# Optimization experiments

Hardware: AMD Instinct MI355X
Metric: run time of the kernel (lower is better)

Reference implementation:

```python
import jax, jax.numpy as jnp
import numpy as np

MOV_DIM = 16
HID = 128
N_MOV = 500_000
N_PHASE = 125_000
N_EDGE = 1_000_000


def setup_inputs() -> dict:
    key = jax.random.key(0)
    ks = jax.random.split(key, 16)
    s_in = 1.0 / np.sqrt(MOV_DIM)
    s_h = 1.0 / np.sqrt(HID)
    inp = {
        "x_movement": jax.random.normal(ks[0], (N_MOV, MOV_DIM), jnp.float32),
        "W1": jax.random.normal(ks[1], (MOV_DIM, HID), jnp.float32) * s_in,
        "b1": jnp.full((HID,), 0.01, jnp.float32),
        "W2": jax.random.normal(ks[2], (HID, HID), jnp.float32) * s_h,
        "b2": jnp.full((HID,), 0.01, jnp.float32),
        "W3": jax.random.normal(ks[3], (HID, HID), jnp.float32) * s_h,
        "b3": jnp.full((HID,), 0.01, jnp.float32),
        "W4": jax.random.normal(ks[4], (HID, HID), jnp.float32) * s_h,
        "b4": jnp.full((HID,), 0.01, jnp.float32),
        "W5": jax.random.normal(ks[5], (HID, HID), jnp.float32) * s_h,
        "b5": jnp.full((HID,), 0.01, jnp.float32),
        "W6": jax.random.normal(ks[6], (HID, 1), jnp.float32) * s_h,
        "b6": jnp.full((1,), 0.01, jnp.float32),
        "edge_src": jax.random.randint(ks[7], (N_EDGE,), 0, N_MOV, jnp.int32),
        "edge_dst": jax.random.randint(ks[8], (N_EDGE,), 0, N_PHASE, jnp.int32),
        "n_phases": N_PHASE,
    }
    return inp


def reference(x_movement, W1, b1, W2, b2, W3, b3, W4, b4, W5, b5, W6, b6,
              edge_src, edge_dst, n_phases):
    h = jax.nn.relu(x_movement @ W1 + b1)
    h = jax.nn.relu(h @ W2 + b2)
    h = jax.nn.relu(h @ W3 + b3)
    # scatter-mean aggregation movement -> phase over edge list
    msg = h[edge_src]                                   # [E, HID] gather
    ssum = jax.ops.segment_sum(msg, edge_dst, num_segments=n_phases)
    cnt = jax.ops.segment_sum(jnp.ones((edge_dst.shape[0],), h.dtype),
                              edge_dst, num_segments=n_phases)
    agg = ssum / jnp.maximum(cnt, 1.0)[:, None]          # [N_phase, HID]
    # phase MLP -> logits
    p = jax.nn.relu(agg @ W4 + b4)
    p = jax.nn.relu(p @ W5 + b5)
    logits = (p @ W6 + b6).squeeze(-1)                  # [N_phase]
    return logits
```

## Files before the change

kernel.cpp:

```cpp
#include <hip/hip_runtime.h>
#include <hip/hip_bf16.h>


typedef __attribute__((ext_vector_type(8))) short short8;
typedef __attribute__((ext_vector_type(4))) float f32x4;

union U8 { short8 s8; unsigned int u[4]; };

__device__ __forceinline__ float bf2f(unsigned short u) {
  return __uint_as_float(((unsigned int)u) << 16);
}
__device__ __forceinline__ unsigned short f2bf(float f) {
  unsigned int u = __float_as_uint(f);
  u = (u + 0x7fffu + ((u >> 16) & 1u)) >> 16;
  return (unsigned short)u;
}
__device__ __forceinline__ unsigned int pk2(float a, float b) {
  __hip_bfloat162 h = __float22bfloat162_rn(make_float2(a, b));
  unsigned int u;
  __builtin_memcpy(&u, &h, 4);
  return u;
}

__global__ __launch_bounds__(256)
void prep_weights(const float* __restrict__ W1, const float* __restrict__ W2,
                  const float* __restrict__ W3, const float* __restrict__ W4,
                  const float* __restrict__ W5,
                  unsigned short* __restrict__ w1t, unsigned short* __restrict__ w2t,
                  unsigned short* __restrict__ w3t, unsigned short* __restrict__ w4t,
                  unsigned short* __restrict__ w5t) {
  int t = blockIdx.x * blockDim.x + threadIdx.x;
  int stride = gridDim.x * blockDim.x;
  if (t < 128 * 32) {
    int c = t >> 5, k = t & 31;
    w1t[t] = (k < 16) ? f2bf(W1[k * 128 + c]) : 0;
  }
  for (int i = t; i < 128 * 128; i += stride) {
    int c = i >> 7, k = i & 127;
    w2t[i] = f2bf(W2[k * 128 + c]);
    w3t[i] = f2bf(W3[k * 128 + c]);
    w4t[i] = f2bf(W4[k * 128 + c]);
    w5t[i] = f2bf(W5[k * 128 + c]);
  }
}

__device__ __forceinline__
void mov_tile(int rowBlk, unsigned short* sH,
              const float* __restrict__ x,
              const unsigned short* __restrict__ w1t,
              const unsigned short* __restrict__ w2t,
              const unsigned short* __restrict__ w3t,
              const float* __restrict__ b1, const float* __restrict__ b2,
              const float* __restrict__ b3,
              unsigned short* __restrict__ hout, int nrows) {
  const int tid  = threadIdx.x;
  const int lane = tid & 63;
  const int w    = tid >> 6;
  const int li   = lane & 15;
  const int g    = lane >> 4;
  const int r0w  = (w & 1) * 32;
  const int c0   = (w >> 1) * 64;

  f32x4 acc[2][4];
  short8 Bf[4][4];

#pragma unroll
  for (int cf = 0; cf < 4; ++cf) {
    float4 b4 = *(const float4*)&b1[c0 + cf * 16 + g * 4];
#pragma unroll
    for (int rf = 0; rf < 2; ++rf) {
      acc[rf][cf][0] = b4.x; acc[rf][cf][1] = b4.y;
      acc[rf][cf][2] = b4.z; acc[rf][cf][3] = b4.w;
    }
  }
  {
    short8 Ax[2];
#pragma unroll
    for (int rf = 0; rf < 2; ++rf) {
      U8 a; a.s8 = (short8)0;
      int row = rowBlk + r0w + rf * 16 + li;
      if (g < 2 && row < nrows) {
        const float* xp = x + (size_t)row * 16 + g * 8;
        float4 u0 = *(const float4*)xp;
        float4 u1 = *(const float4*)(xp + 4);
        a.u[0] = pk2(u0.x, u0.y); a.u[1] = pk2(u0.z, u0.w);
        a.u[2] = pk2(u1.x, u1.y); a.u[3] = pk2(u1.z, u1.w);
      }
      Ax[rf] = a.s8;
    }
    short8 B1[4];
#pragma unroll
    for (int cf = 0; cf < 4; ++cf)
      B1[cf] = *(const short8*)&w1t[(c0 + cf * 16 + li) * 32 + g * 8];
#pragma unroll
    for (int rf = 0; rf < 2; ++rf)
#pragma unroll
      for (int cf = 0; cf < 4; ++cf)
        acc[rf][cf] = __builtin_amdgcn_mfma_f32_16x16x32_bf16(B1[cf], Ax[rf], acc[rf][cf], 0, 0, 0);
  }

#pragma unroll
  for (int rf = 0; rf < 2; ++rf) {
    int s = r0w + rf * 16 + li;
    unsigned short* dst = &sH[s * 128 + (g & 1) * 4];
    int sx = s & 7;
#pragma unroll
    for (int cf = 0; cf < 4; ++cf) {
      int gi = (c0 >> 3) + cf * 2 + (g >> 1);
      int slot = gi ^ sx;
      uint2 u;
      u.x = pk2(fmaxf(acc[rf][cf][0], 0.f), fmaxf(acc[rf][cf][1], 0.f));
      u.y = pk2(fmaxf(acc[rf][cf][2], 0.f), fmaxf(acc[rf][cf][3], 0.f));
      *(uint2*)(dst + slot * 8) = u;
    }
  }
  __syncthreads();

  const unsigned short* wts[2] = { w2t, w3t };
  const float* bs[2] = { b2, b3 };
#pragma unroll 1
  for (int layer = 0; layer < 2; ++layer) {
    const unsigned short* wt = wts[layer];
    const float* bb = bs[layer];
#pragma unroll
    for (int ks = 0; ks < 4; ++ks)
#pragma unroll
      for (int cf = 0; cf < 4; ++cf)
        Bf[ks][cf] = *(const short8*)&wt[(c0 + cf * 16 + li) * 128 + ks * 32 + g * 8];

#pragma unroll
    for (int cf = 0; cf < 4; ++cf) {
      float4 b4 = *(const float4*)&bb[c0 + cf * 16 + g * 4];
#pragma unroll
      for (int rf = 0; rf < 2; ++rf) {
        acc[rf][cf][0] = b4.x; acc[rf][cf][1] = b4.y;
        acc[rf][cf][2] = b4.z; acc[rf][cf][3] = b4.w;
      }
    }

#pragma unroll
    for (int ks = 0; ks < 4; ++ks) {
      short8 Ar[2];
#pragma unroll
      for (int rf = 0; rf < 2; ++rf) {
        int s = r0w + rf * 16 + li;
        int slot = (ks * 4 + g) ^ (s & 7);
        Ar[rf] = *(const short8*)&sH[s * 128 + slot * 8];
      }
#pragma unroll
      for (int rf = 0; rf < 2; ++rf)
#pragma unroll
        for (int cf = 0; cf < 4; ++cf)
          acc[rf][cf] = __builtin_amdgcn_mfma_f32_16x16x32_bf16(Bf[ks][cf], Ar[rf], acc[rf][cf], 0, 0, 0);
    }
    __syncthreads();

#pragma unroll
    for (int rf = 0; rf < 2; ++rf) {
      int s = r0w + rf * 16 + li;
      unsigned short* dst = &sH[s * 128 + (g & 1) * 4];
      int sx = s & 7;
#pragma unroll
      for (int cf = 0; cf < 4; ++cf) {
        int gi = (c0 >> 3) + cf * 2 + (g >> 1);
        int slot = gi ^ sx;
        uint2 u;
        u.x = pk2(fmaxf(acc[rf][cf][0], 0.f), fmaxf(acc[rf][cf][1], 0.f));
        u.y = pk2(fmaxf(acc[rf][cf][2], 0.f), fmaxf(acc[rf][cf][3], 0.f));
        *(uint2*)(dst + slot * 8) = u;
      }
    }
    __syncthreads();
  }

  {
    int r = tid >> 2;
    int q = tid & 3;
    int grow = rowBlk + r;
    if (grow < nrows) {
#pragma unroll
      for (int i = 0; i < 4; ++i) {
        int gi = q * 4 + i;
        int slot = gi ^ (r & 7);
        short8 v = *(const short8*)&sH[r * 128 + slot * 8];
        *(short8*)(hout + (size_t)grow * 128 + gi * 8) = v;
      }
    }
  }
}

__device__ __forceinline__ bool role_other(int b, int k, int otherB, int* oIdx, int* mIdx) {
  bool other = ((b % k) == (k - 1)) && ((b / k) < otherB);
  *oIdx = b / k;
  int before = min((b + 1) / k, otherB);
  *mIdx = b - before;
  return other;
}

__global__ __launch_bounds__(256)
void mov_hist_kernel(const float* __restrict__ x,
                     const unsigned short* __restrict__ w1t,
                     const unsigned short* __restrict__ w2t,
                     const unsigned short* __restrict__ w3t,
                     const float* __restrict__ b1, const float* __restrict__ b2,
                     const float* __restrict__ b3,
                     unsigned short* __restrict__ hout, int nrows,
                     const int* __restrict__ edst, int* __restrict__ cnt, int ne,
                     int k, int histB) {
  __shared__ unsigned short sH[64 * 128];
  int oIdx, mIdx;
  if (role_other(blockIdx.x, k, histB, &oIdx, &mIdx)) {
    int i = oIdx * 256 + threadIdx.x;
    int stride = histB * 256;
    for (int e = i; e < ne; e += stride) atomicAdd(cnt + edst[e], 1);
    return;
  }
  mov_tile(mIdx * 64, sH, x, w1t, w2t, w3t, b1, b2, b3, hout, nrows);
}

__global__ __launch_bounds__(256)
void mov_fill_kernel(const float* __restrict__ x,
                     const unsigned short* __restrict__ w1t,
                     const unsigned short* __restrict__ w2t,
                     const unsigned short* __restrict__ w3t,
                     const float* __restrict__ b1, const float* __restrict__ b2,
                     const float* __restrict__ b3,
                     unsigned short* __restrict__ hout, int nrows, int movABlocks,
                     const int* __restrict__ esrc, const int* __restrict__ edst,
                     int* __restrict__ cursor, int* __restrict__ csr, int ne,
                     int k, int fillB) {
  __shared__ unsigned short sH[64 * 128];
  int oIdx, mIdx;
  if (role_other(blockIdx.x, k, fillB, &oIdx, &mIdx)) {
    int i = oIdx * 256 + threadIdx.x;
    int stride = fillB * 256;
    for (int e = i; e < ne; e += stride) {
      int d = edst[e];
      int pos = atomicAdd(cursor + d, 1);
      csr[pos] = esrc[e];
    }
    return;
  }
  mov_tile((movABlocks + mIdx) * 64, sH, x, w1t, w2t, w3t, b1, b2, b3, hout, nrows);
}

__global__ __launch_bounds__(256)
void scan_sum_kernel(const int* __restrict__ cnt, int* __restrict__ bsum, int nph) {
  __shared__ int red[256];
  const int b = blockIdx.x, t = threadIdx.x;
  const int base = b * 1024 + t * 4;
  int s = 0;
#pragma unroll
  for (int i = 0; i < 4; ++i) {
    int idx = base + i;
    if (idx < nph) s += cnt[idx];
  }
  red[t] = s;
  __syncthreads();
  for (int d = 128; d > 0; d >>= 1) {
    if (t < d) red[t] += red[t + d];
    __syncthreads();
  }
  if (t == 0) bsum[b] = red[0];
}

__global__ __launch_bounds__(256)
void scan_top_kernel(const int* __restrict__ bsum, int* __restrict__ boff,
                     int* __restrict__ offs_end, int nb) {
  __shared__ int part[256];
  const int t = threadIdx.x;
  part[t] = (t < nb) ? bsum[t] : 0;
  __syncthreads();
  for (int d = 1; d < 256; d <<= 1) {
    int v = (t >= d) ? part[t - d] : 0;
    __syncthreads();
    part[t] += v;
    __syncthreads();
  }
  if (t < nb) boff[t] = (t == 0) ? 0 : part[t - 1];
  if (t == 255) *offs_end = part[255];
}

__global__ __launch_bounds__(256)
void scan_fill_kernel(const int* __restrict__ cnt, const int* __restrict__ boff,
                      int* __restrict__ offs, int* __restrict__ cursor, int nph) {
  __shared__ int part[256];
  const int b = blockIdx.x, t = threadIdx.x;
  const int base = b * 1024 + t * 4;
  int v[4];
  int s = 0;
#pragma unroll
  for (int i = 0; i < 4; ++i) {
    int idx = base + i;
    v[i] = (idx < nph) ? cnt[idx] : 0;
    s += v[i];
  }
  part[t] = s;
  __syncthreads();
  for (int d = 1; d < 256; d <<= 1) {
    int u = (t >= d) ? part[t - d] : 0;
    __syncthreads();
    part[t] += u;
    __syncthreads();
  }
  int run = boff[b] + ((t == 0) ? 0 : part[t - 1]);
#pragma unroll
  for (int i = 0; i < 4; ++i) {
    int idx = base + i;
    if (idx < nph) {
      offs[idx] = run;
      cursor[idx] = run;
      run += v[i];
    }
  }
}

__global__ __launch_bounds__(256)
void agg_kernel(const unsigned short* __restrict__ h, const int* __restrict__ csr,
                const int* __restrict__ offs, unsigned short* __restrict__ agg,
                int nph) {
  const int grp = threadIdx.x >> 5;
  const int l   = threadIdx.x & 31;
  const int ph  = blockIdx.x * 8 + grp;
  if (ph >= nph) return;
  const int beg = offs[ph], end = offs[ph + 1];

  f32x4 a0 = (f32x4)0.f, a1 = (f32x4)0.f, a2 = (f32x4)0.f, a3 = (f32x4)0.f;
  int j = beg;
  for (; j + 4 <= end; j += 4) {
    int s0 = csr[j], s1 = csr[j + 1], s2 = csr[j + 2], s3 = csr[j + 3];
    ushort4 v0 = *(const ushort4*)(h + (size_t)s0 * 128 + l * 4);
    ushort4 v1 = *(const ushort4*)(h + (size_t)s1 * 128 + l * 4);
    ushort4 v2 = *(const ushort4*)(h + (size_t)s2 * 128 + l * 4);
    ushort4 v3 = *(const ushort4*)(h + (size_t)s3 * 128 + l * 4);
    a0[0] += bf2f(v0.x); a0[1] += bf2f(v0.y); a0[2] += bf2f(v0.z); a0[3] += bf2f(v0.w);
    a1[0] += bf2f(v1.x); a1[1] += bf2f(v1.y); a1[2] += bf2f(v1.z); a1[3] += bf2f(v1.w);
    a2[0] += bf2f(v2.x); a2[1] += bf2f(v2.y); a2[2] += bf2f(v2.z); a2[3] += bf2f(v2.w);
    a3[0] += bf2f(v3.x); a3[1] += bf2f(v3.y); a3[2] += bf2f(v3.z); a3[3] += bf2f(v3.w);
  }
  for (; j < end; ++j) {
    int s = csr[j];
    ushort4 v = *(const ushort4*)(h + (size_t)s * 128 + l * 4);
    a0[0] += bf2f(v.x); a0[1] += bf2f(v.y); a0[2] += bf2f(v.z); a0[3] += bf2f(v.w);
  }
  const float sc = 1.f / (float)max(end - beg, 1);
  ushort4 o;
  o.x = f2bf((a0[0] + a1[0] + a2[0] + a3[0]) * sc);
  o.y = f2bf((a0[1] + a1[1] + a2[1] + a3[1]) * sc);
  o.z = f2bf((a0[2] + a1[2] + a2[2] + a3[2]) * sc);
  o.w = f2bf((a0[3] + a1[3] + a2[3] + a3[3]) * sc);
  *(ushort4*)(agg + (size_t)ph * 128 + l * 4) = o;
}

__global__ __launch_bounds__(256)
void phase_mlp_mfma(const unsigned short* __restrict__ aggb,
                    const unsigned short* __restrict__ w4t,
                    const unsigned short* __restrict__ w5t,
                    const float* __restrict__ b4, const float* __restrict__ b5,
                    const float* __restrict__ W6, const float* __restrict__ b6,
                    float* __restrict__ logits, int nph) {
  __shared__ unsigned short sH[64 * 128];
  float* sPart = (float*)sH;
  const int tid  = threadIdx.x;
  const int lane = tid & 63;
  const int w    = tid >> 6;
  const int rloc = lane & 15;
  const int g    = lane >> 4;
  const int r0w  = (w & 1) * 32;
  const int c0   = (w >> 1) * 64;
  const int rowBlk = blockIdx.x * 64;

  f32x4 acc[2][4];
  short8 Bf[4][4];

#pragma unroll
  for (int ks = 0; ks < 4; ++ks)
#pragma unroll
    for (int cf = 0; cf < 4; ++cf)
      Bf[ks][cf] = *(const short8*)&w4t[(c0 + cf * 16 + rloc) * 128 + ks * 32 + g * 8];
#pragma unroll
  for (int rf = 0; rf < 2; ++rf)
#pragma unroll
    for (int cf = 0; cf < 4; ++cf) acc[rf][cf] = (f32x4)0.f;

  {
    const int row0 = rowBlk + r0w + rloc;
    const int row1 = row0 + 16;
#pragma unroll
    for (int ks = 0; ks < 4; ++ks) {
      short8 A0 = (short8)0, A1 = (short8)0;
      if (row0 < nph) A0 = *(const short8*)&aggb[(size_t)row0 * 128 + ks * 32 + g * 8];
      if (row1 < nph) A1 = *(const short8*)&aggb[(size_t)row1 * 128 + ks * 32 + g * 8];
#pragma unroll
      for (int cf = 0; cf < 4; ++cf) {
        acc[0][cf] = __builtin_amdgcn_mfma_f32_16x16x32_bf16(A0, Bf[ks][cf], acc[0][cf], 0, 0, 0);
        acc[1][cf] = __builtin_amdgcn_mfma_f32_16x16x32_bf16(A1, Bf[ks][cf], acc[1][cf], 0, 0, 0);
      }
    }
  }

  {
    float bv[4];
#pragma unroll
    for (int cf = 0; cf < 4; ++cf) bv[cf] = b4[c0 + cf * 16 + rloc];
#pragma unroll
    for (int rf = 0; rf < 2; ++rf)
#pragma unroll
      for (int cf = 0; cf < 4; ++cf)
#pragma unroll
        for (int i = 0; i < 4; ++i) {
          int row = r0w + rf * 16 + g * 4 + i;
          int col = c0 + cf * 16 + rloc;
          float v = fmaxf(acc[rf][cf][i] + bv[cf], 0.f);
          sH[row * 128 + (((col >> 3) ^ (row & 7)) << 3) + (col & 7)] = f2bf(v);
        }
  }
  __syncthreads();

#pragma unroll
  for (int ks = 0; ks < 4; ++ks)
#pragma unroll
    for (int cf = 0; cf < 4; ++cf)
      Bf[ks][cf] = *(const short8*)&w5t[(c0 + cf * 16 + rloc) * 128 + ks * 32 + g * 8];
#pragma unroll
  for (int rf = 0; rf < 2; ++rf)
#pragma unroll
    for (int cf = 0; cf < 4; ++cf) acc[rf][cf] = (f32x4)0.f;

#pragma unroll
  for (int ks = 0; ks < 4; ++ks) {
    short8 A0, A1;
    {
      int row = r0w + rloc;
      int slot = (ks * 4 + g) ^ (row & 7);
      A0 = *(const short8*)&sH[row * 128 + slot * 8];
    }
    {
      int row = r0w + 16 + rloc;
      int slot = (ks * 4 + g) ^ (row & 7);
      A1 = *(const short8*)&sH[row * 128 + slot * 8];
    }
#pragma unroll
    for (int cf = 0; cf < 4; ++cf) {
      acc[0][cf] = __builtin_amdgcn_mfma_f32_16x16x32_bf16(A0, Bf[ks][cf], acc[0][cf], 0, 0, 0);
      acc[1][cf] = __builtin_amdgcn_mfma_f32_16x16x32_bf16(A1, Bf[ks][cf], acc[1][cf], 0, 0, 0);
    }
  }

  float part8[2][4];
  {
    float bv[4], wv[4];
#pragma unroll
    for (int cf = 0; cf < 4; ++cf) {
      bv[cf] = b5[c0 + cf * 16 + rloc];
      wv[cf] = W6[c0 + cf * 16 + rloc];
    }
#pragma unroll
    for (int rf = 0; rf < 2; ++rf)
#pragma unroll
      for (int i = 0; i < 4; ++i) {
        float p = 0.f;
#pragma unroll
        for (int cf = 0; cf < 4; ++cf)
          p += fmaxf(acc[rf][cf][i] + bv[cf], 0.f) * wv[cf];
        part8[rf][i] = p;
      }
  }
#pragma unroll
  for (int m = 1; m < 16; m <<= 1) {
#pragma unroll
    for (int rf = 0; rf < 2; ++rf)
#pragma unroll
      for (int i = 0; i < 4; ++i)
        part8[rf][i] += __shfl_xor(part8[rf][i], m, 64);
  }
  __syncthreads();
  if (rloc == 0) {
#pragma unroll
    for (int rf = 0; rf < 2; ++rf)
#pragma unroll
      for (int i = 0; i < 4; ++i)
        sPart[(w >> 1) * 64 + r0w + rf * 16 + g * 4 + i] = part8[rf][i];
  }
  __syncthreads();
  if (tid < 64) {
    int gr = rowBlk + tid;
    if (gr < nph) logits[gr] = sPart[tid] + sPart[64 + tid] + b6[0];
  }
}

extern "C" void kernel_launch(void* const* d_in, const int* in_sizes, int n_in,
                              void* d_out, int out_size, void* d_ws, size_t ws_size,
                              hipStream_t stream) {
  const float* x  = (const float*)d_in[0];
  const float* W1 = (const float*)d_in[1];
  const float* b1 = (const float*)d_in[2];
  const float* W2 = (const float*)d_in[3];
  const float* b2 = (const float*)d_in[4];
  const float* W3 = (const float*)d_in[5];
  const float* b3 = (const float*)d_in[6];
  const float* W4 = (const float*)d_in[7];
  const float* b4 = (const float*)d_in[8];
  const float* W5 = (const float*)d_in[9];
  const float* b5 = (const float*)d_in[10];
  const float* W6 = (const float*)d_in[11];
  const float* b6 = (const float*)d_in[12];
  const int* esrc = (const int*)d_in[13];
  const int* edst = (const int*)d_in[14];

  const int nmov = in_sizes[0] / 16;
  const int ne   = in_sizes[13];
  const int nph  = out_size;

  char* ws = (char*)d_ws;
  size_t off = 0;
  auto take = [&](size_t bytes) {
    char* p = ws + off;
    off = (off + bytes + 255) & ~(size_t)255;
    return p;
  };
  unsigned short* hbuf = (unsigned short*)take((size_t)nmov * 128 * 2);
  int* csr             = (int*)take((size_t)ne * 4);
  int* cnt             = (int*)take((size_t)nph * 4);
  int* offs            = (int*)take(((size_t)nph + 1) * 4);
  int* cursor          = (int*)take((size_t)nph * 4);
  unsigned short* aggb = (unsigned short*)take((size_t)nph * 128 * 2);
  unsigned short* w1t  = (unsigned short*)take(128 * 32 * 2);
  unsigned short* w2t  = (unsigned short*)take(128 * 128 * 2);
  unsigned short* w3t  = (unsigned short*)take(128 * 128 * 2);
  unsigned short* w4t  = (unsigned short*)take(128 * 128 * 2);
  unsigned short* w5t  = (unsigned short*)take(128 * 128 * 2);
  const int nb = (nph + 1023) / 1024;
  int* bsum            = (int*)take((size_t)nb * 4);
  int* boff            = (int*)take((size_t)nb * 4);
  if (off > ws_size) return;

  (void)hipMemsetAsync(cnt, 0, (size_t)nph * 4, stream);

  prep_weights<<<64, 256, 0, stream>>>(W1, W2, W3, W4, W5, w1t, w2t, w3t, w4t, w5t);

  const int movBlocks = (nmov + 63) / 64;
  const int movA = (movBlocks * 5) / 8;
  const int movB = movBlocks - movA;

  const int histB = 1024;
  {
    const int N1 = movA + histB;
    int k1 = N1 / histB;
    if (k1 < 2) k1 = 2;
    mov_hist_kernel<<<N1, 256, 0, stream>>>(
        x, w1t, w2t, w3t, b1, b2, b3, hbuf, nmov, edst, cnt, ne, k1, histB);
  }

  scan_sum_kernel<<<nb, 256, 0, stream>>>(cnt, bsum, nph);
  scan_top_kernel<<<1, 256, 0, stream>>>(bsum, boff, offs + nph, nb);
  scan_fill_kernel<<<nb, 256, 0, stream>>>(cnt, boff, offs, cursor, nph);

  const int fillB = 1024;
  {
    const int N2 = movB + fillB;
    int k2 = N2 / fillB;
    if (k2 < 2) k2 = 2;
    mov_fill_kernel<<<N2, 256, 0, stream>>>(
        x, w1t, w2t, w3t, b1, b2, b3, hbuf, nmov, movA,
        esrc, edst, cursor, csr, ne, k2, fillB);
  }

  int aggBlocks = (nph + 7) / 8;
  agg_kernel<<<aggBlocks, 256, 0, stream>>>(hbuf, csr, offs, aggb, nph);

  int phBlocks = (nph + 63) / 64;
  phase_mlp_mfma<<<phBlocks, 256, 0, stream>>>(aggb, w4t, w5t, b4, b5, W6, b6,
                                               (float*)d_out, nph);
}
```

Measured before the change: 293.4 us.

## Fuse scatter-mean aggregation into phase MLP and merge scan/memset launches

Each phase-MLP block now gathers and averages its own 64 phase rows from the CSR straight into swizzled shared memory, so the agg kernel and the global bf16 agg buffer round trip are gone. The top-level scan is folded into scan_fill (every block redundantly scans the block sums), and zeroing the counts moves into prep_weights, replacing the memset. This removes several launches and some global traffic. In exchange the fused kernel runs far fewer blocks during the memory-latency-bound gather (phBlocks vs aggBlocks), which may reduce latency hiding.

```diff
diff --git a/kernel.cpp b/kernel.cpp
--- a/kernel.cpp
+++ b/kernel.cpp
@@ -28,7 +28,8 @@
                   const float* __restrict__ W5,
                   unsigned short* __restrict__ w1t, unsigned short* __restrict__ w2t,
                   unsigned short* __restrict__ w3t, unsigned short* __restrict__ w4t,
-                  unsigned short* __restrict__ w5t) {
+                  unsigned short* __restrict__ w5t,
+                  int* __restrict__ cnt, int nph) {
   int t = blockIdx.x * blockDim.x + threadIdx.x;
   int stride = gridDim.x * blockDim.x;
   if (t < 128 * 32) {
@@ -42,6 +43,7 @@
     w4t[i] = f2bf(W4[k * 128 + c]);
     w5t[i] = f2bf(W5[k * 128 + c]);
   }
+  for (int i = t; i < nph; i += stride) cnt[i] = 0;
 }
 
 __device__ __forceinline__
@@ -265,27 +267,23 @@
 }
 
 __global__ __launch_bounds__(256)
-void scan_top_kernel(const int* __restrict__ bsum, int* __restrict__ boff,
-                     int* __restrict__ offs_end, int nb) {
-  __shared__ int part[256];
-  const int t = threadIdx.x;
-  part[t] = (t < nb) ? bsum[t] : 0;
-  __syncthreads();
-  for (int d = 1; d < 256; d <<= 1) {
-    int v = (t >= d) ? part[t - d] : 0;
-    __syncthreads();
-    part[t] += v;
-    __syncthreads();
-  }
-  if (t < nb) boff[t] = (t == 0) ? 0 : part[t - 1];
-  if (t == 255) *offs_end = part[255];
-}
-
-__global__ __launch_bounds__(256)
-void scan_fill_kernel(const int* __restrict__ cnt, const int* __restrict__ boff,
-                      int* __restrict__ offs, int* __restrict__ cursor, int nph) {
+void scan_fill_kernel(const int* __restrict__ cnt, const int* __restrict__ bsum,
+                      int* __restrict__ offs, int* __restrict__ cursor,
+                      int nph, int nb) {
+  __shared__ int top[256];
   __shared__ int part[256];
   const int b = blockIdx.x, t = threadIdx.x;
+  top[t] = (t < nb) ? bsum[t] : 0;
+  __syncthreads();
+  for (int d = 1; d < 256; d <<= 1) {
+    int v = (t >= d) ? top[t - d] : 0;
+    __syncthreads();
+    top[t] += v;
+    __syncthreads();
+  }
+  const int blockBase = (b == 0) ? 0 : top[b - 1];
+  if (b == 0 && t == 0) offs[nph] = top[nb - 1];
+
   const int base = b * 1024 + t * 4;
   int v[4];
   int s = 0;
@@ -303,7 +301,7 @@
     part[t] += u;
     __syncthreads();
   }
-  int run = boff[b] + ((t == 0) ? 0 : part[t - 1]);
+  int run = blockBase + ((t == 0) ? 0 : part[t - 1]);
 #pragma unroll
   for (int i = 0; i < 4; ++i) {
     int idx = base + i;
@@ -316,59 +314,68 @@
 }
 
 __global__ __launch_bounds__(256)
-void agg_kernel(const unsigned short* __restrict__ h, const int* __restrict__ csr,
-                const int* __restrict__ offs, unsigned short* __restrict__ agg,
-                int nph) {
-  const int grp = threadIdx.x >> 5;
-  const int l   = threadIdx.x & 31;
-  const int ph  = blockIdx.x * 8 + grp;
-  if (ph >= nph) return;
-  const int beg = offs[ph], end = offs[ph + 1];
-
-  f32x4 a0 = (f32x4)0.f, a1 = (f32x4)0.f, a2 = (f32x4)0.f, a3 = (f32x4)0.f;
-  int j = beg;
-  for (; j + 4 <= end; j += 4) {
-    int s0 = csr[j], s1 = csr[j + 1], s2 = csr[j + 2], s3 = csr[j + 3];
-    ushort4 v0 = *(const ushort4*)(h + (size_t)s0 * 128 + l * 4);
-    ushort4 v1 = *(const ushort4*)(h + (size_t)s1 * 128 + l * 4);
-    ushort4 v2 = *(const ushort4*)(h + (size_t)s2 * 128 + l * 4);
-    ushort4 v3 = *(const ushort4*)(h + (size_t)s3 * 128 + l * 4);
-    a0[0] += bf2f(v0.x); a0[1] += bf2f(v0.y); a0[2] += bf2f(v0.z); a0[3] += bf2f(v0.w);
-    a1[0] += bf2f(v1.x); a1[1] += bf2f(v1.y); a1[2] += bf2f(v1.z); a1[3] += bf2f(v1.w);
-    a2[0] += bf2f(v2.x); a2[1] += bf2f(v2.y); a2[2] += bf2f(v2.z); a2[3] += bf2f(v2.w);
-    a3[0] += bf2f(v3.x); a3[1] += bf2f(v3.y); a3[2] += bf2f(v3.z); a3[3] += bf2f(v3.w);
-  }
-  for (; j < end; ++j) {
-    int s = csr[j];
-    ushort4 v = *(const ushort4*)(h + (size_t)s * 128 + l * 4);
-    a0[0] += bf2f(v.x); a0[1] += bf2f(v.y); a0[2] += bf2f(v.z); a0[3] += bf2f(v.w);
-  }
-  const float sc = 1.f / (float)max(end - beg, 1);
-  ushort4 o;
-  o.x = f2bf((a0[0] + a1[0] + a2[0] + a3[0]) * sc);
-  o.y = f2bf((a0[1] + a1[1] + a2[1] + a3[1]) * sc);
-  o.z = f2bf((a0[2] + a1[2] + a2[2] + a3[2]) * sc);
-  o.w = f2bf((a0[3] + a1[3] + a2[3] + a3[3]) * sc);
-  *(ushort4*)(agg + (size_t)ph * 128 + l * 4) = o;
-}
-
-__global__ __launch_bounds__(256)
-void phase_mlp_mfma(const unsigned short* __restrict__ aggb,
-                    const unsigned short* __restrict__ w4t,
-                    const unsigned short* __restrict__ w5t,
-                    const float* __restrict__ b4, const float* __restrict__ b5,
-                    const float* __restrict__ W6, const float* __restrict__ b6,
-                    float* __restrict__ logits, int nph) {
+void phase_fused(const unsigned short* __restrict__ h, const int* __restrict__ csr,
+                 const int* __restrict__ offs,
+                 const unsigned short* __restrict__ w4t,
+                 const unsigned short* __restrict__ w5t,
+                 const float* __restrict__ b4, const float* __restrict__ b5,
+                 const float* __restrict__ W6, const float* __restrict__ b6,
+                 float* __restrict__ logits, int nph) {
   __shared__ unsigned short sH[64 * 128];
   float* sPart = (float*)sH;
   const int tid  = threadIdx.x;
+  const int rowBlk = blockIdx.x * 64;
+
+  {
+    const int grp = tid >> 5;
+    const int l   = tid & 31;
+#pragma unroll 1
+    for (int p = 0; p < 8; ++p) {
+      int lrow = grp * 8 + p;
+      int ph = rowBlk + lrow;
+      float c0v = 0.f, c1v = 0.f, c2v = 0.f, c3v = 0.f;
+      if (ph < nph) {
+        const int beg = offs[ph], end = offs[ph + 1];
+        f32x4 a0 = (f32x4)0.f, a1 = (f32x4)0.f, a2 = (f32x4)0.f, a3 = (f32x4)0.f;
+        int j = beg;
+        for (; j + 4 <= end; j += 4) {
+          int s0 = csr[j], s1 = csr[j + 1], s2 = csr[j + 2], s3 = csr[j + 3];
+          ushort4 v0 = *(const ushort4*)(h + (size_t)s0 * 128 + l * 4);
+          ushort4 v1 = *(const ushort4*)(h + (size_t)s1 * 128 + l * 4);
+          ushort4 v2 = *(const ushort4*)(h + (size_t)s2 * 128 + l * 4);
+          ushort4 v3 = *(const ushort4*)(h + (size_t)s3 * 128 + l * 4);
+          a0[0] += bf2f(v0.x); a0[1] += bf2f(v0.y); a0[2] += bf2f(v0.z); a0[3] += bf2f(v0.w);
+          a1[0] += bf2f(v1.x); a1[1] += bf2f(v1.y); a1[2] += bf2f(v1.z); a1[3] += bf2f(v1.w);
+          a2[0] += bf2f(v2.x); a2[1] += bf2f(v2.y); a2[2] += bf2f(v2.z); a2[3] += bf2f(v2.w);
+          a3[0] += bf2f(v3.x); a3[1] += bf2f(v3.y); a3[2] += bf2f(v3.z); a3[3] += bf2f(v3.w);
+        }
+        for (; j < end; ++j) {
+          int s = csr[j];
+          ushort4 v = *(const ushort4*)(h + (size_t)s * 128 + l * 4);
+          a0[0] += bf2f(v.x); a0[1] += bf2f(v.y); a0[2] += bf2f(v.z); a0[3] += bf2f(v.w);
+        }
+        const float sc = 1.f / (float)max(end - beg, 1);
+        c0v = (a0[0] + a1[0] + a2[0] + a3[0]) * sc;
+        c1v = (a0[1] + a1[1] + a2[1] + a3[1]) * sc;
+        c2v = (a0[2] + a1[2] + a2[2] + a3[2]) * sc;
+        c3v = (a0[3] + a1[3] + a2[3] + a3[3]) * sc;
+      }
+      int gi = l >> 1;
+      int slot = gi ^ (lrow & 7);
+      uint2 u;
+      u.x = pk2(c0v, c1v);
+      u.y = pk2(c2v, c3v);
+      *(uint2*)&sH[lrow * 128 + slot * 8 + (l & 1) * 4] = u;
+    }
+  }
+  __syncthreads();
+
   const int lane = tid & 63;
   const int w    = tid >> 6;
   const int rloc = lane & 15;
   const int g    = lane >> 4;
   const int r0w  = (w & 1) * 32;
   const int c0   = (w >> 1) * 64;
-  const int rowBlk = blockIdx.x * 64;
 
   f32x4 acc[2][4];
   short8 Bf[4][4];
@@ -383,21 +390,26 @@
 #pragma unroll
     for (int cf = 0; cf < 4; ++cf) acc[rf][cf] = (f32x4)0.f;
 
-  {
-    const int row0 = rowBlk + r0w + rloc;
-    const int row1 = row0 + 16;
-#pragma unroll
-    for (int ks = 0; ks < 4; ++ks) {
-      short8 A0 = (short8)0, A1 = (short8)0;
-      if (row0 < nph) A0 = *(const short8*)&aggb[(size_t)row0 * 128 + ks * 32 + g * 8];
-      if (row1 < nph) A1 = *(const short8*)&aggb[(size_t)row1 * 128 + ks * 32 + g * 8];
-#pragma unroll
-      for (int cf = 0; cf < 4; ++cf) {
-        acc[0][cf] = __builtin_amdgcn_mfma_f32_16x16x32_bf16(A0, Bf[ks][cf], acc[0][cf], 0, 0, 0);
-        acc[1][cf] = __builtin_amdgcn_mfma_f32_16x16x32_bf16(A1, Bf[ks][cf], acc[1][cf], 0, 0, 0);
-      }
-    }
-  }
+#pragma unroll
+  for (int ks = 0; ks < 4; ++ks) {
+    short8 A0, A1;
+    {
+      int row = r0w + rloc;
+      int slot = (ks * 4 + g) ^ (row & 7);
+      A0 = *(const short8*)&sH[row * 128 + slot * 8];
+    }
+    {
+      int row = r0w + 16 + rloc;
+      int slot = (ks * 4 + g) ^ (row & 7);
+      A1 = *(const short8*)&sH[row * 128 + slot * 8];
+    }
+#pragma unroll
+    for (int cf = 0; cf < 4; ++cf) {
+      acc[0][cf] = __builtin_amdgcn_mfma_f32_16x16x32_bf16(A0, Bf[ks][cf], acc[0][cf], 0, 0, 0);
+      acc[1][cf] = __builtin_amdgcn_mfma_f32_16x16x32_bf16(A1, Bf[ks][cf], acc[1][cf], 0, 0, 0);
+    }
+  }
+  __syncthreads();
 
   {
     float bv[4];
@@ -524,7 +536,6 @@
   int* cnt             = (int*)take((size_t)nph * 4);
   int* offs            = (int*)take(((size_t)nph + 1) * 4);
   int* cursor          = (int*)take((size_t)nph * 4);
-  unsigned short* aggb = (unsigned short*)take((size_t)nph * 128 * 2);
   unsigned short* w1t  = (unsigned short*)take(128 * 32 * 2);
   unsigned short* w2t  = (unsigned short*)take(128 * 128 * 2);
   unsigned short* w3t  = (unsigned short*)take(128 * 128 * 2);
@@ -532,12 +543,10 @@
   unsigned short* w5t  = (unsigned short*)take(128 * 128 * 2);
   const int nb = (nph + 1023) / 1024;
   int* bsum            = (int*)take((size_t)nb * 4);
-  int* boff            = (int*)take((size_t)nb * 4);
   if (off > ws_size) return;
 
-  (void)hipMemsetAsync(cnt, 0, (size_t)nph * 4, stream);
-
-  prep_weights<<<64, 256, 0, stream>>>(W1, W2, W3, W4, W5, w1t, w2t, w3t, w4t, w5t);
+  prep_weights<<<64, 256, 0, stream>>>(W1, W2, W3, W4, W5,
+                                       w1t, w2t, w3t, w4t, w5t, cnt, nph);
 
   const int movBlocks = (nmov + 63) / 64;
   const int movA = (movBlocks * 5) / 8;
@@ -553,8 +562,7 @@
   }
 
   scan_sum_kernel<<<nb, 256, 0, stream>>>(cnt, bsum, nph);
-  scan_top_kernel<<<1, 256, 0, stream>>>(bsum, boff, offs + nph, nb);
-  scan_fill_kernel<<<nb, 256, 0, stream>>>(cnt, boff, offs, cursor, nph);
+  scan_fill_kernel<<<nb, 256, 0, stream>>>(cnt, bsum, offs, cursor, nph, nb);
 
   const int fillB = 1024;
   {
@@ -566,10 +574,7 @@
         esrc, edst, cursor, csr, ne, k2, fillB);
   }
 
-  int aggBlocks = (nph + 7) / 8;
-  agg_kernel<<<aggBlocks, 256, 0, stream>>>(hbuf, csr, offs, aggb, nph);
-
   int phBlocks = (nph + 63) / 64;
-  phase_mlp_mfma<<<phBlocks, 256, 0, stream>>>(aggb, w4t, w5t, b4, b5, W6, b6,
-                                               (float*)d_out, nph);
-}
+  phase_fused<<<phBlocks, 256, 0, stream>>>(hbuf, csr, offs, w4t, w5t,
+                                            b4, b5, W6, b6, (float*)d_out, nph);
+}
```

Result: no change. 296.3 us (+1.0%).
